# Optimization experiments

Measured on AMD Instinct MI355X. Metric: run time of the kernel, lower is better.

## Reference

```python
import jax, jax.numpy as jnp
import numpy as np

HIDDEN = 256
NUM_FEATURE = 64
N_ROWS = 100000
N_EDGES = 400000

def setup_inputs() -> dict:
    key = jax.random.key(0)
    ks = jax.random.split(key, 12)
    inp = {}
    # forward args
    inp["known_mask"] = (jax.random.uniform(ks[0], (N_ROWS, NUM_FEATURE)) > 0.5).astype(jnp.float32)
    inp["obs_idx"] = jax.random.randint(ks[1], (N_EDGES,), 0, N_ROWS)
    inp["obs_mask_idx"] = jax.random.randint(ks[2], (N_EDGES,), 0, N_ROWS)
    inp["attr_idx_need_to_be_impute"] = jax.random.randint(ks[3], (N_EDGES,), 0, NUM_FEATURE)
    inp["obs_embs"] = jax.random.normal(ks[4], (N_ROWS, HIDDEN), dtype=jnp.float32)
    inp["feature_emb"] = jax.random.normal(ks[5], (NUM_FEATURE, HIDDEN), dtype=jnp.float32)
    # learned params (phi_rm: F->H->F, phi_rr: F->H, phi_rc: H->H)
    s = 0.05
    inp["rm_W1"] = jax.random.normal(ks[6], (NUM_FEATURE, HIDDEN), dtype=jnp.float32) * s
    inp["rm_b1"] = jnp.zeros((HIDDEN,), jnp.float32)
    inp["rm_W2"] = jax.random.normal(ks[7], (HIDDEN, NUM_FEATURE), dtype=jnp.float32) * s
    inp["rm_b2"] = jnp.zeros((NUM_FEATURE,), jnp.float32)
    inp["rr_W"] = jax.random.normal(ks[8], (NUM_FEATURE, HIDDEN), dtype=jnp.float32) * s
    inp["rr_b"] = jnp.zeros((HIDDEN,), jnp.float32)
    inp["rc_W"] = jax.random.normal(ks[9], (HIDDEN, HIDDEN), dtype=jnp.float32) * s
    inp["rc_b"] = jnp.zeros((HIDDEN,), jnp.float32)
    return inp

def _gelu(x):
    return jax.nn.gelu(x, approximate=False)  # torch nn.GELU default = exact erf

def reference(known_mask, obs_idx, obs_mask_idx, attr_idx_need_to_be_impute,
              obs_embs, feature_emb,
              rm_W1, rm_b1, rm_W2, rm_b2, rr_W, rr_b, rc_W, rc_b):
    F_ = feature_emb.shape[0]
    self_mask = 1.0 - jnp.eye(F_, dtype=known_mask.dtype)
    obs_h = obs_embs[obs_idx]                                # [E, H]
    target = feature_emb[attr_idx_need_to_be_impute]          # [E, H]
    m_i = known_mask[obs_mask_idx]                            # [E, F]
    m_j = self_mask[attr_idx_need_to_be_impute]               # [E, F]
    # batched [1,H] @ [H,F] == single GEMM [E,H] @ [H,F]
    a_j_i = target @ feature_emb.T                            # [E, F]
    m_J_I = jax.nn.softmax(m_i * m_j, axis=1)                 # [E, F]
    m_J_I = _gelu(_gelu(m_J_I @ rm_W1 + rm_b1) @ rm_W2 + rm_b2)  # phi_rm
    a_j_i = _gelu((a_j_i * m_J_I) @ rr_W + rr_b)              # phi_rr -> [E, H]
    c_r_ji = _gelu((obs_h * a_j_i) @ rc_W + rc_b)             # phi_rc (dropout=eval identity)
    return c_r_ji
```

## Files before the change

### kernel.cpp

```cpp
#include <hip/hip_runtime.h>
#include <hip/hip_bf16.h>

typedef __bf16 bf16;
typedef float f32x4 __attribute__((ext_vector_type(4)));
typedef bf16 bf16x8 __attribute__((ext_vector_type(8)));
typedef bf16 bf16x4 __attribute__((ext_vector_type(4)));

#define E_TOT 400000
#define TE 64
#define SROW 264

__device__ __forceinline__ float gelu_exact(float x){
  float z = fabsf(x) * 0.70710678118654752f;
  float t = __builtin_amdgcn_rcpf(__builtin_fmaf(0.3275911f, z, 1.0f));
  float p = __builtin_fmaf(1.061405429f, t, -1.453152027f);
  p = __builtin_fmaf(p, t, 1.421413741f);
  p = __builtin_fmaf(p, t, -0.284496736f);
  p = __builtin_fmaf(p, t, 0.254829592f);
  p = p * t;
  float ex = __expf(-z * z);
  float er = __builtin_fmaf(-p, ex, 1.0f);
  er = copysignf(er, x);
  return 0.5f * x * (1.0f + er);
}

__device__ __forceinline__ float gelu_fast(float x){
  float x2 = x * x;
  float y  = x * __builtin_fmaf(0.07135482f, x2, 1.5957691216f);
  float e  = __expf(y);
  float r  = __builtin_amdgcn_rcpf(e + 1.0f);
  return __builtin_fmaf(-x, r, x);
}

__global__ void compute_g(const float* __restrict__ fe, float* __restrict__ Gm){
  const int a = blockIdx.x, f = threadIdx.x;
  const float4* ra = (const float4*)(fe + a * 256);
  const float4* rf = (const float4*)(fe + f * 256);
  float s = 0.f;
  for (int h = 0; h < 64; ++h){
    float4 x = ra[h];
    float4 y = rf[h];
    s += x.x * y.x + x.y * y.y + x.z * y.z + x.w * y.w;
  }
  Gm[a * 64 + f] = s;
}

__global__ void swizzle_w(const float* __restrict__ src, bf16* __restrict__ dst,
                          int Kd, int Md){
  const int t = blockIdx.x;
  const int L = threadIdx.x;
  const int Mtiles = Md >> 4;
  const int kt = t / Mtiles, mtg = t % Mtiles;
  const int k0 = kt * 32 + (L >> 4) * 8;
  const int m  = mtg * 16 + (L & 15);
  bf16x8 v;
  #pragma unroll
  for (int j = 0; j < 8; ++j) v[j] = (bf16)src[(k0 + j) * Md + m];
  *(bf16x8*)&dst[((size_t)t * 64 + L) * 8] = v;
}

template<int KT, int MT, int MTOT>
__device__ __forceinline__ void mfma_gemm(const bf16* __restrict__ Wz,
                                          const bf16* __restrict__ src,
                                          int w, int lane,
                                          const float4 (&binit)[MT],
                                          f32x4 (&acc)[MT][4])
{
  const int l16 = lane & 15, quad = lane >> 4;
  #pragma unroll
  for (int mt = 0; mt < MT; ++mt)
    #pragma unroll
    for (int et = 0; et < 4; ++et)
      acc[mt][et] = f32x4{binit[mt].x, binit[mt].y, binit[mt].z, binit[mt].w};
  #pragma unroll
  for (int kt = 0; kt < KT; ++kt){
    bf16x8 b[4];
    #pragma unroll
    for (int et = 0; et < 4; ++et)
      b[et] = *(const bf16x8*)&src[(et * 16 + l16) * SROW + kt * 32 + quad * 8];
    #pragma unroll
    for (int mt = 0; mt < MT; ++mt){
      const bf16x8 a = *(const bf16x8*)&Wz[(size_t)((kt * MTOT + (w * MT + mt)) * 64 + lane) * 8];
      #pragma unroll
      for (int et = 0; et < 4; ++et)
        acc[mt][et] = __builtin_amdgcn_mfma_f32_16x16x32_bf16(a, b[et], acc[mt][et], 0, 0, 0);
    }
  }
}

__global__ __launch_bounds__(256, 4) void fused_attr_net(
    const float* __restrict__ km,
    const int*   __restrict__ obs_idx,
    const int*   __restrict__ omi_idx,
    const int*   __restrict__ ai_idx,
    const float* __restrict__ obs_embs,
    const float* __restrict__ b1g, const float* __restrict__ b2g,
    const float* __restrict__ rrbg, const float* __restrict__ rcbg,
    const float* __restrict__ Gm,
    const bf16* __restrict__ W1s, const bf16* __restrict__ W2s,
    const bf16* __restrict__ RRs, const bf16* __restrict__ RCs,
    float* __restrict__ out)
{
  __shared__ __align__(16) bf16 S_[TE * SROW];
  __shared__ int ai_s[TE];
  __shared__ int oi_s[TE];
  __shared__ __align__(16) float bias1[256];
  __shared__ __align__(16) float bias2[64];
  __shared__ __align__(16) float biasrr[256];
  __shared__ __align__(16) float biasrc[256];

  const int tid  = threadIdx.x;
  const int e0   = blockIdx.x * TE;
  const int lane = tid & 63;
  const int w    = tid >> 6;
  const int l16  = lane & 15;
  const int quad = lane >> 4;

  bias1[tid]  = b1g[tid];
  biasrr[tid] = rrbg[tid];
  biasrc[tid] = rcbg[tid];
  if (tid < TE){
    bias2[tid] = b2g[tid];
    ai_s[tid]  = ai_idx[e0 + tid];
    oi_s[tid]  = obs_idx[e0 + tid];
  }

  {
    const int e = tid >> 2, part = tid & 3;
    const int omi = omi_idx[e0 + e];
    const int ai  = ai_idx[e0 + e];
    const float4* kr = (const float4*)(km + omi * 64 + part * 16);
    float s[16]; float cnt = 0.f;
    #pragma unroll
    for (int q = 0; q < 4; ++q){
      const float4 v4 = kr[q];
      const float vv[4] = {v4.x, v4.y, v4.z, v4.w};
      #pragma unroll
      for (int j = 0; j < 4; ++j){
        const int f = part * 16 + q * 4 + j;
        const float v = (f == ai) ? 0.f : vv[j];
        s[q * 4 + j] = v; cnt += v;
      }
    }
    cnt += __shfl_xor(cnt, 1);
    cnt += __shfl_xor(cnt, 2);
    const float denom = __builtin_fmaf(cnt, 1.7182818284590452f, 64.0f);
    const float p0 = __builtin_amdgcn_rcpf(denom);
    const float d10 = 1.7182818284590452f * p0;
    bf16x8 o0, o1;
    #pragma unroll
    for (int j = 0; j < 8; ++j) o0[j] = (bf16)__builtin_fmaf(s[j],     d10, p0);
    #pragma unroll
    for (int j = 0; j < 8; ++j) o1[j] = (bf16)__builtin_fmaf(s[8 + j], d10, p0);
    *(bf16x8*)&S_[e * SROW + part * 16]     = o0;
    *(bf16x8*)&S_[e * SROW + part * 16 + 8] = o1;
  }
  __syncthreads();

  f32x4 acc[4][4];
  float4 binit4[4];
  float4 binit1[1];

  #pragma unroll
  for (int mt = 0; mt < 4; ++mt)
    binit4[mt] = *(const float4*)&bias1[(w * 4 + mt) * 16 + quad * 4];
  mfma_gemm<2, 4, 16>(W1s, S_, w, lane, binit4, acc);
  __syncthreads();
  #pragma unroll
  for (int mt = 0; mt < 4; ++mt){
    const int mbase = (w * 4 + mt) * 16 + quad * 4;
    #pragma unroll
    for (int et = 0; et < 4; ++et){
      const int e = et * 16 + l16;
      bf16x4 o;
      o[0] = (bf16)gelu_fast(acc[mt][et][0]);
      o[1] = (bf16)gelu_fast(acc[mt][et][1]);
      o[2] = (bf16)gelu_fast(acc[mt][et][2]);
      o[3] = (bf16)gelu_fast(acc[mt][et][3]);
      *(bf16x4*)&S_[e * SROW + mbase] = o;
    }
  }
  __syncthreads();

  {
    f32x4 acc2[1][4];
    binit1[0] = *(const float4*)&bias2[w * 16 + quad * 4];
    mfma_gemm<8, 1, 4>(W2s, S_, w, lane, binit1, acc2);
    __syncthreads();
    const int mbase = w * 16 + quad * 4;
    #pragma unroll
    for (int et = 0; et < 4; ++et){
      const int e = et * 16 + l16;
      const float4 g = *(const float4*)&Gm[ai_s[e] * 64 + mbase];
      bf16x4 o;
      o[0] = (bf16)(gelu_fast(acc2[0][et][0]) * g.x);
      o[1] = (bf16)(gelu_fast(acc2[0][et][1]) * g.y);
      o[2] = (bf16)(gelu_fast(acc2[0][et][2]) * g.z);
      o[3] = (bf16)(gelu_fast(acc2[0][et][3]) * g.w);
      *(bf16x4*)&S_[e * SROW + mbase] = o;
    }
  }
  __syncthreads();

  #pragma unroll
  for (int mt = 0; mt < 4; ++mt)
    binit4[mt] = *(const float4*)&biasrr[(w * 4 + mt) * 16 + quad * 4];
  mfma_gemm<2, 4, 16>(RRs, S_, w, lane, binit4, acc);
  __syncthreads();
  #pragma unroll
  for (int mt = 0; mt < 4; ++mt){
    const int mbase = (w * 4 + mt) * 16 + quad * 4;
    #pragma unroll
    for (int et = 0; et < 4; ++et){
      const int e = et * 16 + l16;
      const float4 oh = *(const float4*)&obs_embs[(size_t)oi_s[e] * 256 + mbase];
      bf16x4 o;
      o[0] = (bf16)(gelu_fast(acc[mt][et][0]) * oh.x);
      o[1] = (bf16)(gelu_fast(acc[mt][et][1]) * oh.y);
      o[2] = (bf16)(gelu_fast(acc[mt][et][2]) * oh.z);
      o[3] = (bf16)(gelu_fast(acc[mt][et][3]) * oh.w);
      *(bf16x4*)&S_[e * SROW + mbase] = o;
    }
  }
  __syncthreads();

  #pragma unroll
  for (int mt = 0; mt < 4; ++mt)
    binit4[mt] = *(const float4*)&biasrc[(w * 4 + mt) * 16 + quad * 4];
  mfma_gemm<8, 4, 16>(RCs, S_, w, lane, binit4, acc);
  #pragma unroll
  for (int mt = 0; mt < 4; ++mt){
    const int mbase = (w * 4 + mt) * 16 + quad * 4;
    #pragma unroll
    for (int et = 0; et < 4; ++et){
      const int e = et * 16 + l16;
      float4 o;
      o.x = gelu_exact(acc[mt][et][0]);
      o.y = gelu_exact(acc[mt][et][1]);
      o.z = gelu_exact(acc[mt][et][2]);
      o.w = gelu_exact(acc[mt][et][3]);
      *(float4*)&out[(size_t)(e0 + e) * 256 + mbase] = o;
    }
  }
}

extern "C" void kernel_launch(void* const* d_in, const int* in_sizes, int n_in,
                              void* d_out, int out_size, void* d_ws, size_t ws_size,
                              hipStream_t stream){
  const float* km   = (const float*)d_in[0];
  const int*   obsi = (const int*)d_in[1];
  const int*   omi  = (const int*)d_in[2];
  const int*   ai   = (const int*)d_in[3];
  const float* obs  = (const float*)d_in[4];
  const float* fe   = (const float*)d_in[5];
  const float* W1   = (const float*)d_in[6];
  const float* b1   = (const float*)d_in[7];
  const float* W2   = (const float*)d_in[8];
  const float* b2   = (const float*)d_in[9];
  const float* rrW  = (const float*)d_in[10];
  const float* rrb  = (const float*)d_in[11];
  const float* rcW  = (const float*)d_in[12];
  const float* rcb  = (const float*)d_in[13];
  float* out = (float*)d_out;

  char* ws = (char*)d_ws;
  float* Gm  = (float*)ws;
  bf16* W1s  = (bf16*)(ws + 16384);
  bf16* W2s  = (bf16*)(ws + 49152);
  bf16* RRs  = (bf16*)(ws + 81920);
  bf16* RCs  = (bf16*)(ws + 114688);

  compute_g<<<dim3(64), dim3(64), 0, stream>>>(fe, Gm);
  swizzle_w<<<dim3(32),  dim3(64), 0, stream>>>(W1,  W1s, 64,  256);
  swizzle_w<<<dim3(32),  dim3(64), 0, stream>>>(W2,  W2s, 256, 64);
  swizzle_w<<<dim3(32),  dim3(64), 0, stream>>>(rrW, RRs, 64,  256);
  swizzle_w<<<dim3(128), dim3(64), 0, stream>>>(rcW, RCs, 256, 256);
  fused_attr_net<<<dim3(E_TOT / TE), dim3(256), 0, stream>>>(
      km, obsi, omi, ai, obs, b1, b2, rrb, rcb, Gm, W1s, W2s, RRs, RCs, out);
}
```

Before: 715.6 us.

## Give each wave its own 16-edge tile with XOR-swizzled LDS, drop block barriers

Result: slower. 1.100 ms (+53.7%).

```diff
diff --git a/kernel.cpp b/kernel.cpp
--- a/kernel.cpp
+++ b/kernel.cpp
@@ -8,7 +8,6 @@
 
 #define E_TOT 400000
 #define TE 64
-#define SROW 264
 
 __device__ __forceinline__ float gelu_exact(float x){
   float z = fabsf(x) * 0.70710678118654752f;
@@ -59,36 +58,29 @@
   *(bf16x8*)&dst[((size_t)t * 64 + L) * 8] = v;
 }
 
-template<int KT, int MT, int MTOT>
+template<int KT, int MT>
 __device__ __forceinline__ void mfma_gemm(const bf16* __restrict__ Wz,
-                                          const bf16* __restrict__ src,
-                                          int w, int lane,
-                                          const float4 (&binit)[MT],
-                                          f32x4 (&acc)[MT][4])
+                                          const bf16* __restrict__ Sw,
+                                          const float* __restrict__ bias,
+                                          int lane, f32x4 (&acc)[MT])
 {
   const int l16 = lane & 15, quad = lane >> 4;
   #pragma unroll
   for (int mt = 0; mt < MT; ++mt)
-    #pragma unroll
-    for (int et = 0; et < 4; ++et)
-      acc[mt][et] = f32x4{binit[mt].x, binit[mt].y, binit[mt].z, binit[mt].w};
+    acc[mt] = *(const f32x4*)&bias[mt * 16 + quad * 4];
   #pragma unroll
   for (int kt = 0; kt < KT; ++kt){
-    bf16x8 b[4];
-    #pragma unroll
-    for (int et = 0; et < 4; ++et)
-      b[et] = *(const bf16x8*)&src[(et * 16 + l16) * SROW + kt * 32 + quad * 8];
+    const int col = (kt * 32 + quad * 8) ^ ((l16 & 7) << 3);
+    const bf16x8 b = *(const bf16x8*)&Sw[l16 * 256 + col];
     #pragma unroll
     for (int mt = 0; mt < MT; ++mt){
-      const bf16x8 a = *(const bf16x8*)&Wz[(size_t)((kt * MTOT + (w * MT + mt)) * 64 + lane) * 8];
-      #pragma unroll
-      for (int et = 0; et < 4; ++et)
-        acc[mt][et] = __builtin_amdgcn_mfma_f32_16x16x32_bf16(a, b[et], acc[mt][et], 0, 0, 0);
+      const bf16x8 a = *(const bf16x8*)&Wz[(size_t)((kt * MT + mt) * 64 + lane) * 8];
+      acc[mt] = __builtin_amdgcn_mfma_f32_16x16x32_bf16(a, b, acc[mt], 0, 0, 0);
     }
   }
 }
 
-__global__ __launch_bounds__(256, 4) void fused_attr_net(
+__global__ __launch_bounds__(256, 5) void fused_attr_net(
     const float* __restrict__ km,
     const int*   __restrict__ obs_idx,
     const int*   __restrict__ omi_idx,
@@ -101,13 +93,7 @@
     const bf16* __restrict__ RRs, const bf16* __restrict__ RCs,
     float* __restrict__ out)
 {
-  __shared__ __align__(16) bf16 S_[TE * SROW];
-  __shared__ int ai_s[TE];
-  __shared__ int oi_s[TE];
-  __shared__ __align__(16) float bias1[256];
-  __shared__ __align__(16) float bias2[64];
-  __shared__ __align__(16) float biasrr[256];
-  __shared__ __align__(16) float biasrc[256];
+  __shared__ __align__(16) bf16 S_[4 * 16 * 256];
 
   const int tid  = threadIdx.x;
   const int e0   = blockIdx.x * TE;
@@ -115,20 +101,19 @@
   const int w    = tid >> 6;
   const int l16  = lane & 15;
   const int quad = lane >> 4;
-
-  bias1[tid]  = b1g[tid];
-  biasrr[tid] = rrbg[tid];
-  biasrc[tid] = rcbg[tid];
-  if (tid < TE){
-    bias2[tid] = b2g[tid];
-    ai_s[tid]  = ai_idx[e0 + tid];
-    oi_s[tid]  = obs_idx[e0 + tid];
-  }
+  const int swz  = (l16 & 7) << 3;
+
+  bf16* Sw = S_ + w * 16 * 256;
+
+  const int myedge = e0 + w * 16 + l16;
+  const int aiv = ai_idx[myedge];
+  const int oiv = obs_idx[myedge];
 
   {
-    const int e = tid >> 2, part = tid & 3;
-    const int omi = omi_idx[e0 + e];
-    const int ai  = ai_idx[e0 + e];
+    const int eL = lane >> 2, part = lane & 3;
+    const int edge = e0 + w * 16 + eL;
+    const int omi = omi_idx[edge];
+    const int ai  = ai_idx[edge];
     const float4* kr = (const float4*)(km + omi * 64 + part * 16);
     float s[16]; float cnt = 0.f;
     #pragma unroll
@@ -152,95 +137,64 @@
     for (int j = 0; j < 8; ++j) o0[j] = (bf16)__builtin_fmaf(s[j],     d10, p0);
     #pragma unroll
     for (int j = 0; j < 8; ++j) o1[j] = (bf16)__builtin_fmaf(s[8 + j], d10, p0);
-    *(bf16x8*)&S_[e * SROW + part * 16]     = o0;
-    *(bf16x8*)&S_[e * SROW + part * 16 + 8] = o1;
-  }
-  __syncthreads();
-
-  f32x4 acc[4][4];
-  float4 binit4[4];
-  float4 binit1[1];
-
-  #pragma unroll
-  for (int mt = 0; mt < 4; ++mt)
-    binit4[mt] = *(const float4*)&bias1[(w * 4 + mt) * 16 + quad * 4];
-  mfma_gemm<2, 4, 16>(W1s, S_, w, lane, binit4, acc);
-  __syncthreads();
-  #pragma unroll
-  for (int mt = 0; mt < 4; ++mt){
-    const int mbase = (w * 4 + mt) * 16 + quad * 4;
-    #pragma unroll
-    for (int et = 0; et < 4; ++et){
-      const int e = et * 16 + l16;
+    const int sw = (eL & 7) << 3;
+    *(bf16x8*)&Sw[eL * 256 + ((part * 16)     ^ sw)] = o0;
+    *(bf16x8*)&Sw[eL * 256 + ((part * 16 + 8) ^ sw)] = o1;
+  }
+
+  f32x4 acc[16];
+
+  mfma_gemm<2, 16>(W1s, Sw, b1g, lane, acc);
+  #pragma unroll
+  for (int mt = 0; mt < 16; ++mt){
+    const int c = (mt * 16 + quad * 4) ^ swz;
+    bf16x4 o;
+    o[0] = (bf16)gelu_fast(acc[mt][0]);
+    o[1] = (bf16)gelu_fast(acc[mt][1]);
+    o[2] = (bf16)gelu_fast(acc[mt][2]);
+    o[3] = (bf16)gelu_fast(acc[mt][3]);
+    *(bf16x4*)&Sw[l16 * 256 + c] = o;
+  }
+
+  {
+    f32x4 acc2[4];
+    mfma_gemm<8, 4>(W2s, Sw, b2g, lane, acc2);
+    #pragma unroll
+    for (int mt = 0; mt < 4; ++mt){
+      const int m0 = mt * 16 + quad * 4;
+      const float4 g = *(const float4*)&Gm[aiv * 64 + m0];
       bf16x4 o;
-      o[0] = (bf16)gelu_fast(acc[mt][et][0]);
-      o[1] = (bf16)gelu_fast(acc[mt][et][1]);
-      o[2] = (bf16)gelu_fast(acc[mt][et][2]);
-      o[3] = (bf16)gelu_fast(acc[mt][et][3]);
-      *(bf16x4*)&S_[e * SROW + mbase] = o;
+      o[0] = (bf16)(gelu_fast(acc2[mt][0]) * g.x);
+      o[1] = (bf16)(gelu_fast(acc2[mt][1]) * g.y);
+      o[2] = (bf16)(gelu_fast(acc2[mt][2]) * g.z);
+      o[3] = (bf16)(gelu_fast(acc2[mt][3]) * g.w);
+      *(bf16x4*)&Sw[l16 * 256 + (m0 ^ swz)] = o;
     }
   }
-  __syncthreads();
-
-  {
-    f32x4 acc2[1][4];
-    binit1[0] = *(const float4*)&bias2[w * 16 + quad * 4];
-    mfma_gemm<8, 1, 4>(W2s, S_, w, lane, binit1, acc2);
-    __syncthreads();
-    const int mbase = w * 16 + quad * 4;
-    #pragma unroll
-    for (int et = 0; et < 4; ++et){
-      const int e = et * 16 + l16;
-      const float4 g = *(const float4*)&Gm[ai_s[e] * 64 + mbase];
-      bf16x4 o;
-      o[0] = (bf16)(gelu_fast(acc2[0][et][0]) * g.x);
-      o[1] = (bf16)(gelu_fast(acc2[0][et][1]) * g.y);
-      o[2] = (bf16)(gelu_fast(acc2[0][et][2]) * g.z);
-      o[3] = (bf16)(gelu_fast(acc2[0][et][3]) * g.w);
-      *(bf16x4*)&S_[e * SROW + mbase] = o;
-    }
-  }
-  __syncthreads();
-
-  #pragma unroll
-  for (int mt = 0; mt < 4; ++mt)
-    binit4[mt] = *(const float4*)&biasrr[(w * 4 + mt) * 16 + quad * 4];
-  mfma_gemm<2, 4, 16>(RRs, S_, w, lane, binit4, acc);
-  __syncthreads();
-  #pragma unroll
-  for (int mt = 0; mt < 4; ++mt){
-    const int mbase = (w * 4 + mt) * 16 + quad * 4;
-    #pragma unroll
-    for (int et = 0; et < 4; ++et){
-      const int e = et * 16 + l16;
-      const float4 oh = *(const float4*)&obs_embs[(size_t)oi_s[e] * 256 + mbase];
-      bf16x4 o;
-      o[0] = (bf16)(gelu_fast(acc[mt][et][0]) * oh.x);
-      o[1] = (bf16)(gelu_fast(acc[mt][et][1]) * oh.y);
-      o[2] = (bf16)(gelu_fast(acc[mt][et][2]) * oh.z);
-      o[3] = (bf16)(gelu_fast(acc[mt][et][3]) * oh.w);
-      *(bf16x4*)&S_[e * SROW + mbase] = o;
-    }
-  }
-  __syncthreads();
-
-  #pragma unroll
-  for (int mt = 0; mt < 4; ++mt)
-    binit4[mt] = *(const float4*)&biasrc[(w * 4 + mt) * 16 + quad * 4];
-  mfma_gemm<8, 4, 16>(RCs, S_, w, lane, binit4, acc);
-  #pragma unroll
-  for (int mt = 0; mt < 4; ++mt){
-    const int mbase = (w * 4 + mt) * 16 + quad * 4;
-    #pragma unroll
-    for (int et = 0; et < 4; ++et){
-      const int e = et * 16 + l16;
-      float4 o;
-      o.x = gelu_exact(acc[mt][et][0]);
-      o.y = gelu_exact(acc[mt][et][1]);
-      o.z = gelu_exact(acc[mt][et][2]);
-      o.w = gelu_exact(acc[mt][et][3]);
-      *(float4*)&out[(size_t)(e0 + e) * 256 + mbase] = o;
-    }
+
+  mfma_gemm<2, 16>(RRs, Sw, rrbg, lane, acc);
+  #pragma unroll
+  for (int mt = 0; mt < 16; ++mt){
+    const int m0 = mt * 16 + quad * 4;
+    const float4 oh = *(const float4*)&obs_embs[(size_t)oiv * 256 + m0];
+    bf16x4 o;
+    o[0] = (bf16)(gelu_fast(acc[mt][0]) * oh.x);
+    o[1] = (bf16)(gelu_fast(acc[mt][1]) * oh.y);
+    o[2] = (bf16)(gelu_fast(acc[mt][2]) * oh.z);
+    o[3] = (bf16)(gelu_fast(acc[mt][3]) * oh.w);
+    *(bf16x4*)&Sw[l16 * 256 + (m0 ^ swz)] = o;
+  }
+
+  mfma_gemm<8, 16>(RCs, Sw, rcbg, lane, acc);
+  #pragma unroll
+  for (int mt = 0; mt < 16; ++mt){
+    const int m0 = mt * 16 + quad * 4;
+    float4 o;
+    o.x = gelu_exact(acc[mt][0]);
+    o.y = gelu_exact(acc[mt][1]);
+    o.z = gelu_exact(acc[mt][2]);
+    o.w = gelu_exact(acc[mt][3]);
+    *(float4*)&out[(size_t)myedge * 256 + m0] = o;
   }
 }
 
```

## Split edge tile into two halves and interleave GEMMs with epilogues

Applied to the files above, without the earlier changes.

Result: slower. 745.0 us (+4.1%).

```diff
diff --git a/kernel.cpp b/kernel.cpp
--- a/kernel.cpp
+++ b/kernel.cpp
@@ -60,29 +60,28 @@
 }
 
 template<int KT, int MT, int MTOT>
-__device__ __forceinline__ void mfma_gemm(const bf16* __restrict__ Wz,
-                                          const bf16* __restrict__ src,
-                                          int w, int lane,
-                                          const float4 (&binit)[MT],
-                                          f32x4 (&acc)[MT][4])
+__device__ __forceinline__ void mfma_gemm2(const bf16* __restrict__ Wz,
+                                           const bf16* __restrict__ Sh,
+                                           const float4 (&binit)[MT],
+                                           int w, int lane, f32x4 (&acc)[MT][2])
 {
   const int l16 = lane & 15, quad = lane >> 4;
   #pragma unroll
   for (int mt = 0; mt < MT; ++mt)
     #pragma unroll
-    for (int et = 0; et < 4; ++et)
+    for (int et = 0; et < 2; ++et)
       acc[mt][et] = f32x4{binit[mt].x, binit[mt].y, binit[mt].z, binit[mt].w};
   #pragma unroll
   for (int kt = 0; kt < KT; ++kt){
-    bf16x8 b[4];
-    #pragma unroll
-    for (int et = 0; et < 4; ++et)
-      b[et] = *(const bf16x8*)&src[(et * 16 + l16) * SROW + kt * 32 + quad * 8];
+    bf16x8 b[2];
+    #pragma unroll
+    for (int et = 0; et < 2; ++et)
+      b[et] = *(const bf16x8*)&Sh[(et * 16 + l16) * SROW + kt * 32 + quad * 8];
     #pragma unroll
     for (int mt = 0; mt < MT; ++mt){
       const bf16x8 a = *(const bf16x8*)&Wz[(size_t)((kt * MTOT + (w * MT + mt)) * 64 + lane) * 8];
       #pragma unroll
-      for (int et = 0; et < 4; ++et)
+      for (int et = 0; et < 2; ++et)
         acc[mt][et] = __builtin_amdgcn_mfma_f32_16x16x32_bf16(a, b[et], acc[mt][et], 0, 0, 0);
     }
   }
@@ -104,10 +103,6 @@
   __shared__ __align__(16) bf16 S_[TE * SROW];
   __shared__ int ai_s[TE];
   __shared__ int oi_s[TE];
-  __shared__ __align__(16) float bias1[256];
-  __shared__ __align__(16) float bias2[64];
-  __shared__ __align__(16) float biasrr[256];
-  __shared__ __align__(16) float biasrc[256];
 
   const int tid  = threadIdx.x;
   const int e0   = blockIdx.x * TE;
@@ -116,13 +111,12 @@
   const int l16  = lane & 15;
   const int quad = lane >> 4;
 
-  bias1[tid]  = b1g[tid];
-  biasrr[tid] = rrbg[tid];
-  biasrc[tid] = rcbg[tid];
+  bf16* SA = S_;
+  bf16* SB = S_ + 32 * SROW;
+
   if (tid < TE){
-    bias2[tid] = b2g[tid];
-    ai_s[tid]  = ai_idx[e0 + tid];
-    oi_s[tid]  = obs_idx[e0 + tid];
+    ai_s[tid] = ai_idx[e0 + tid];
+    oi_s[tid] = obs_idx[e0 + tid];
   }
 
   {
@@ -157,91 +151,115 @@
   }
   __syncthreads();
 
-  f32x4 acc[4][4];
-  float4 binit4[4];
-  float4 binit1[1];
+  auto epi_h1 = [&](f32x4 (&A)[4][2], bf16* Sh){
+    #pragma unroll
+    for (int mt = 0; mt < 4; ++mt){
+      const int mbase = (w * 4 + mt) * 16 + quad * 4;
+      #pragma unroll
+      for (int et = 0; et < 2; ++et){
+        const int e = et * 16 + l16;
+        bf16x4 o;
+        o[0] = (bf16)gelu_fast(A[mt][et][0]);
+        o[1] = (bf16)gelu_fast(A[mt][et][1]);
+        o[2] = (bf16)gelu_fast(A[mt][et][2]);
+        o[3] = (bf16)gelu_fast(A[mt][et][3]);
+        *(bf16x4*)&Sh[e * SROW + mbase] = o;
+      }
+    }
+  };
+  auto epi_r = [&](f32x4 (&A)[1][2], bf16* Sh, int hb){
+    const int mbase = w * 16 + quad * 4;
+    #pragma unroll
+    for (int et = 0; et < 2; ++et){
+      const int e = et * 16 + l16;
+      const float4 g = *(const float4*)&Gm[ai_s[hb + e] * 64 + mbase];
+      bf16x4 o;
+      o[0] = (bf16)(gelu_fast(A[0][et][0]) * g.x);
+      o[1] = (bf16)(gelu_fast(A[0][et][1]) * g.y);
+      o[2] = (bf16)(gelu_fast(A[0][et][2]) * g.z);
+      o[3] = (bf16)(gelu_fast(A[0][et][3]) * g.w);
+      *(bf16x4*)&Sh[e * SROW + mbase] = o;
+    }
+  };
+  auto epi_p = [&](f32x4 (&A)[4][2], bf16* Sh, int hb){
+    #pragma unroll
+    for (int mt = 0; mt < 4; ++mt){
+      const int mbase = (w * 4 + mt) * 16 + quad * 4;
+      #pragma unroll
+      for (int et = 0; et < 2; ++et){
+        const int e = et * 16 + l16;
+        const float4 oh = *(const float4*)&obs_embs[(size_t)oi_s[hb + e] * 256 + mbase];
+        bf16x4 o;
+        o[0] = (bf16)(gelu_fast(A[mt][et][0]) * oh.x);
+        o[1] = (bf16)(gelu_fast(A[mt][et][1]) * oh.y);
+        o[2] = (bf16)(gelu_fast(A[mt][et][2]) * oh.z);
+        o[3] = (bf16)(gelu_fast(A[mt][et][3]) * oh.w);
+        *(bf16x4*)&Sh[e * SROW + mbase] = o;
+      }
+    }
+  };
+  auto epi_out = [&](f32x4 (&A)[4][2], int hb){
+    #pragma unroll
+    for (int mt = 0; mt < 4; ++mt){
+      const int mbase = (w * 4 + mt) * 16 + quad * 4;
+      #pragma unroll
+      for (int et = 0; et < 2; ++et){
+        const int e = et * 16 + l16;
+        float4 o;
+        o.x = gelu_exact(A[mt][et][0]);
+        o.y = gelu_exact(A[mt][et][1]);
+        o.z = gelu_exact(A[mt][et][2]);
+        o.w = gelu_exact(A[mt][et][3]);
+        *(float4*)&out[(size_t)(e0 + hb + e) * 256 + mbase] = o;
+      }
+    }
+  };
+
+  f32x4 X[4][2], Y[4][2];
+  f32x4 X2[1][2], Y2[1][2];
+  float4 b4[4], b21[1];
 
   #pragma unroll
   for (int mt = 0; mt < 4; ++mt)
-    binit4[mt] = *(const float4*)&bias1[(w * 4 + mt) * 16 + quad * 4];
-  mfma_gemm<2, 4, 16>(W1s, S_, w, lane, binit4, acc);
-  __syncthreads();
-  #pragma unroll
-  for (int mt = 0; mt < 4; ++mt){
-    const int mbase = (w * 4 + mt) * 16 + quad * 4;
-    #pragma unroll
-    for (int et = 0; et < 4; ++et){
-      const int e = et * 16 + l16;
-      bf16x4 o;
-      o[0] = (bf16)gelu_fast(acc[mt][et][0]);
-      o[1] = (bf16)gelu_fast(acc[mt][et][1]);
-      o[2] = (bf16)gelu_fast(acc[mt][et][2]);
-      o[3] = (bf16)gelu_fast(acc[mt][et][3]);
-      *(bf16x4*)&S_[e * SROW + mbase] = o;
-    }
-  }
-  __syncthreads();
-
-  {
-    f32x4 acc2[1][4];
-    binit1[0] = *(const float4*)&bias2[w * 16 + quad * 4];
-    mfma_gemm<8, 1, 4>(W2s, S_, w, lane, binit1, acc2);
-    __syncthreads();
-    const int mbase = w * 16 + quad * 4;
-    #pragma unroll
-    for (int et = 0; et < 4; ++et){
-      const int e = et * 16 + l16;
-      const float4 g = *(const float4*)&Gm[ai_s[e] * 64 + mbase];
-      bf16x4 o;
-      o[0] = (bf16)(gelu_fast(acc2[0][et][0]) * g.x);
-      o[1] = (bf16)(gelu_fast(acc2[0][et][1]) * g.y);
-      o[2] = (bf16)(gelu_fast(acc2[0][et][2]) * g.z);
-      o[3] = (bf16)(gelu_fast(acc2[0][et][3]) * g.w);
-      *(bf16x4*)&S_[e * SROW + mbase] = o;
-    }
-  }
+    b4[mt] = *(const float4*)&b1g[(w * 4 + mt) * 16 + quad * 4];
+  mfma_gemm2<2, 4, 16>(W1s, SA, b4, w, lane, X);
+  __syncthreads();
+
+  epi_h1(X, SA);
+  mfma_gemm2<2, 4, 16>(W1s, SB, b4, w, lane, Y);
+  __syncthreads();
+
+  b21[0] = *(const float4*)&b2g[w * 16 + quad * 4];
+  epi_h1(Y, SB);
+  mfma_gemm2<8, 1, 4>(W2s, SA, b21, w, lane, X2);
+  __syncthreads();
+
+  epi_r(X2, SA, 0);
+  mfma_gemm2<8, 1, 4>(W2s, SB, b21, w, lane, Y2);
   __syncthreads();
 
   #pragma unroll
   for (int mt = 0; mt < 4; ++mt)
-    binit4[mt] = *(const float4*)&biasrr[(w * 4 + mt) * 16 + quad * 4];
-  mfma_gemm<2, 4, 16>(RRs, S_, w, lane, binit4, acc);
-  __syncthreads();
-  #pragma unroll
-  for (int mt = 0; mt < 4; ++mt){
-    const int mbase = (w * 4 + mt) * 16 + quad * 4;
-    #pragma unroll
-    for (int et = 0; et < 4; ++et){
-      const int e = et * 16 + l16;
-      const float4 oh = *(const float4*)&obs_embs[(size_t)oi_s[e] * 256 + mbase];
-      bf16x4 o;
-      o[0] = (bf16)(gelu_fast(acc[mt][et][0]) * oh.x);
-      o[1] = (bf16)(gelu_fast(acc[mt][et][1]) * oh.y);
-      o[2] = (bf16)(gelu_fast(acc[mt][et][2]) * oh.z);
-      o[3] = (bf16)(gelu_fast(acc[mt][et][3]) * oh.w);
-      *(bf16x4*)&S_[e * SROW + mbase] = o;
-    }
-  }
+    b4[mt] = *(const float4*)&rrbg[(w * 4 + mt) * 16 + quad * 4];
+  epi_r(Y2, SB, 32);
+  mfma_gemm2<2, 4, 16>(RRs, SA, b4, w, lane, X);
+  __syncthreads();
+
+  epi_p(X, SA, 0);
+  mfma_gemm2<2, 4, 16>(RRs, SB, b4, w, lane, Y);
   __syncthreads();
 
   #pragma unroll
   for (int mt = 0; mt < 4; ++mt)
-    binit4[mt] = *(const float4*)&biasrc[(w * 4 + mt) * 16 + quad * 4];
-  mfma_gemm<8, 4, 16>(RCs, S_, w, lane, binit4, acc);
-  #pragma unroll
-  for (int mt = 0; mt < 4; ++mt){
-    const int mbase = (w * 4 + mt) * 16 + quad * 4;
-    #pragma unroll
-    for (int et = 0; et < 4; ++et){
-      const int e = et * 16 + l16;
-      float4 o;
-      o.x = gelu_exact(acc[mt][et][0]);
-      o.y = gelu_exact(acc[mt][et][1]);
-      o.z = gelu_exact(acc[mt][et][2]);
-      o.w = gelu_exact(acc[mt][et][3]);
-      *(float4*)&out[(size_t)(e0 + e) * 256 + mbase] = o;
-    }
-  }
+    b4[mt] = *(const float4*)&rcbg[(w * 4 + mt) * 16 + quad * 4];
+  epi_p(Y, SB, 32);
+  mfma_gemm2<8, 4, 16>(RCs, SA, b4, w, lane, X);
+  __syncthreads();
+
+  epi_out(X, 0);
+  mfma_gemm2<8, 4, 16>(RCs, SB, b4, w, lane, Y);
+
+  epi_out(Y, 32);
 }
 
 extern "C" void kernel_launch(void* const* d_in, const int* in_sizes, int n_in,
```
